# Kernel tuning notes

Hardware: AMD Instinct MI355X
Metric: run time of the kernel (lower is better)

The kernel has to match this reference:

```python
import jax, jax.numpy as jnp
import numpy as np

N_HEADS = 16
HID_DIM = 64
INPUT_DIM = 1024
B, L = 4, 1024
NEG = -10000000000.0


def setup_inputs() -> dict:
    key = jax.random.key(0)
    ks = jax.random.split(key, 10)
    d = INPUT_DIM
    h = N_HEADS * HID_DIM
    s = 1.0 / np.sqrt(d)
    return {
        "query": jax.random.normal(ks[0], (B, L, d), dtype=jnp.float32),
        "key": jax.random.normal(ks[1], (B, L, d), dtype=jnp.float32),
        "value": jax.random.normal(ks[2], (B, L, d), dtype=jnp.float32),
        "mask": jax.random.randint(ks[3], (B, 1, L, L), 0, 2, dtype=jnp.int32),
        "wq": jax.random.normal(ks[4], (d, h), dtype=jnp.float32) * s,
        "bq": jnp.zeros((h,), dtype=jnp.float32),
        "wk": jax.random.normal(ks[5], (d, h), dtype=jnp.float32) * s,
        "bk": jnp.zeros((h,), dtype=jnp.float32),
        "wv": jax.random.normal(ks[6], (d, h), dtype=jnp.float32) * s,
        "bv": jnp.zeros((h,), dtype=jnp.float32),
    }


def _split_heads(x):
    # [B, L, H*D] -> [B, H, L, D]
    b, l, _ = x.shape
    return x.reshape(b, l, N_HEADS, HID_DIM).transpose(0, 2, 1, 3)


def reference(query, key, value, mask, wq, bq, wk, bk, wv, bv):
    scale = jnp.sqrt(jnp.float32(HID_DIM))
    Q = _split_heads(query @ wq + bq)   # [B,H,L,D]
    K = _split_heads(key @ wk + bk)
    V = _split_heads(value @ wv + bv)
    energy = jnp.einsum("bhqd,bhkd->bhqk", Q, K) / scale
    energy = jnp.where(mask == 0, jnp.float32(NEG), energy)
    attention = energy  # NOTE: softmax is intentionally skipped, as in the source
    x = jnp.einsum("bhqk,bhkd->bhqd", attention, V)
    x = x.transpose(0, 2, 1, 3).reshape(query.shape[0], -1, N_HEADS * HID_DIM)
    return (attention, x)
```

## Files before the change

### kernel.cpp

```cpp
#include <hip/hip_runtime.h>
#include <stdint.h>
#include <stddef.h>


typedef __attribute__((ext_vector_type(8))) short short8;
typedef __attribute__((ext_vector_type(4))) float f32x4;
typedef __attribute__((ext_vector_type(4))) int i32x4;
typedef __attribute__((ext_vector_type(2))) unsigned int u32x2;

#define MFMA16(a, b, c) __builtin_amdgcn_mfma_f32_16x16x32_bf16(a, b, c, 0, 0, 0)

using gptr_t = const __attribute__((address_space(1))) void*;
using lptr_t = __attribute__((address_space(3))) void*;

#define NEGV -10000000000.0f
#define NEGV_BF16 0xD015u

__device__ __forceinline__ unsigned short f2bf(float f) {
  uint32_t u = __builtin_bit_cast(uint32_t, f);
  u += 0x7FFFu + ((u >> 16) & 1u);
  return (unsigned short)(u >> 16);
}

__global__ __launch_bounds__(256) void k_convert(
    const float* __restrict__ q, const float* __restrict__ k, const float* __restrict__ v,
    unsigned short* __restrict__ oq, unsigned short* __restrict__ ok,
    unsigned short* __restrict__ ov) {
  const int z = blockIdx.z;
  const float* src = z == 0 ? q : z == 1 ? k : v;
  unsigned short* dst = z == 0 ? oq : z == 1 ? ok : ov;
  const size_t idx = ((size_t)blockIdx.x * 256 + threadIdx.x) * 8;
  f32x4 a = *(const f32x4*)(src + idx);
  f32x4 b = *(const f32x4*)(src + idx + 4);
  short8 o;
  o[0] = (short)f2bf(a[0]); o[1] = (short)f2bf(a[1]);
  o[2] = (short)f2bf(a[2]); o[3] = (short)f2bf(a[3]);
  o[4] = (short)f2bf(b[0]); o[5] = (short)f2bf(b[1]);
  o[6] = (short)f2bf(b[2]); o[7] = (short)f2bf(b[3]);
  *(short8*)(dst + idx) = o;
}

__global__ __launch_bounds__(256) void k_wt(
    const float* __restrict__ wq, const float* __restrict__ wk, const float* __restrict__ wv,
    unsigned short* __restrict__ tq, unsigned short* __restrict__ tk,
    unsigned short* __restrict__ tv) {
  const int z = blockIdx.z;
  const float* src = z == 0 ? wq : z == 1 ? wk : wv;
  unsigned short* dst = z == 0 ? tq : z == 1 ? tk : tv;
  __shared__ unsigned short t[64][65];
  const int n0 = blockIdx.x * 64, k0 = blockIdx.y * 64;
#pragma unroll
  for (int i = 0; i < 16; ++i) {
    const int idx = i * 256 + threadIdx.x;
    const int r = idx >> 6, c = idx & 63;
    t[r][c] = f2bf(src[(size_t)(k0 + r) * 1024 + n0 + c]);
  }
  __syncthreads();
#pragma unroll
  for (int i = 0; i < 16; ++i) {
    const int idx = i * 256 + threadIdx.x;
    const int r = idx >> 6, c = idx & 63;
    dst[(size_t)(n0 + r) * 1024 + k0 + c] = t[c][r];
  }
}

__global__ __launch_bounds__(256) void k_gemm(
    const unsigned short* __restrict__ Xq, const unsigned short* __restrict__ Xk,
    const unsigned short* __restrict__ Xv,
    const unsigned short* __restrict__ Wq, const unsigned short* __restrict__ Wk,
    const unsigned short* __restrict__ Wv,
    const float* __restrict__ bq, const float* __restrict__ bk, const float* __restrict__ bv,
    unsigned short* __restrict__ Cq, unsigned short* __restrict__ Ck,
    unsigned short* __restrict__ Cv) {
  const int z = blockIdx.z;
  const unsigned short* X  = z == 0 ? Xq : z == 1 ? Xk : Xv;
  const unsigned short* Wt = z == 0 ? Wq : z == 1 ? Wk : Wv;
  const float* bias        = z == 0 ? bq : z == 1 ? bk : bv;
  unsigned short* C        = z == 0 ? Cq : z == 1 ? Ck : Cv;

  __shared__ unsigned short Ads[128 * 64];
  __shared__ unsigned short Bds[128 * 64];

  const int tid = threadIdx.x;
  const int w = tid >> 6, l = tid & 63;
  const int lr = l & 15, g = l >> 4;
  const int m0 = blockIdx.y * 128, n0 = blockIdx.x * 128;
  const int wm = (w >> 1) * 64, wn = (w & 1) * 64;
  const int srow = tid >> 3, sslot = tid & 7;

  f32x4 acc[4][4];
#pragma unroll
  for (int mi = 0; mi < 4; ++mi)
#pragma unroll
    for (int ni = 0; ni < 4; ++ni) acc[mi][ni] = (f32x4){0.f, 0.f, 0.f, 0.f};

  for (int kt = 0; kt < 16; ++kt) {
    const int kb = kt * 64;
#pragma unroll
    for (int i = 0; i < 4; ++i) {
      const int row = i * 32 + srow;
      const int scol = ((sslot ^ (row & 7)) << 3);
      const unsigned short* ga = X + (size_t)(m0 + row) * 1024 + kb + scol;
      const unsigned short* gb = Wt + (size_t)(n0 + row) * 1024 + kb + scol;
      __builtin_amdgcn_global_load_lds((gptr_t)ga, (lptr_t)&Ads[(i * 32 + w * 8) * 64], 16, 0, 0);
      __builtin_amdgcn_global_load_lds((gptr_t)gb, (lptr_t)&Bds[(i * 32 + w * 8) * 64], 16, 0, 0);
    }
    __syncthreads();
    short8 afr[4][2], bfr[4][2];
#pragma unroll
    for (int t = 0; t < 4; ++t)
#pragma unroll
      for (int ks = 0; ks < 2; ++ks) {
        const int ra = wm + t * 16 + lr;
        afr[t][ks] = *(const short8*)&Ads[ra * 64 + (((ks * 4 + g) ^ (ra & 7)) << 3)];
        const int rb = wn + t * 16 + lr;
        bfr[t][ks] = *(const short8*)&Bds[rb * 64 + (((ks * 4 + g) ^ (rb & 7)) << 3)];
      }
#pragma unroll
    for (int ks = 0; ks < 2; ++ks)
#pragma unroll
      for (int mi = 0; mi < 4; ++mi)
#pragma unroll
        for (int ni = 0; ni < 4; ++ni)
          acc[mi][ni] = MFMA16(afr[mi][ks], bfr[ni][ks], acc[mi][ni]);
    __syncthreads();
  }

#pragma unroll
  for (int mi = 0; mi < 4; ++mi)
#pragma unroll
    for (int ni = 0; ni < 4; ++ni) {
      const int n = n0 + wn + ni * 16 + lr;
      const float bs = bias[n];
      f32x4 a = acc[mi][ni];
#pragma unroll
      for (int r = 0; r < 4; ++r) {
        const int m = m0 + wm + mi * 16 + g * 4 + r;
        C[(size_t)m * 1024 + n] = f2bf(a[r] + bs);
      }
    }
}

__global__ __launch_bounds__(256) void k_vt(const unsigned short* __restrict__ Vb,
                                            unsigned short* __restrict__ Vt) {
  const int bh = blockIdx.y, b = bh >> 4, h = bh & 15;
  const int l0 = blockIdx.x * 64;
  __shared__ unsigned short t[64][65];
#pragma unroll
  for (int i = 0; i < 16; ++i) {
    const int idx = i * 256 + threadIdx.x;
    const int r = idx >> 6, c = idx & 63;
    t[r][c] = Vb[(size_t)(b * 1024 + l0 + r) * 1024 + h * 64 + c];
  }
  __syncthreads();
#pragma unroll
  for (int i = 0; i < 16; ++i) {
    const int idx = i * 256 + threadIdx.x;
    const int r = idx >> 6, c = idx & 63;
    Vt[(size_t)(bh * 64 + r) * 1024 + l0 + c] = t[c][r];
  }
}

__global__ __launch_bounds__(512, 4) void k_attn(
    const unsigned short* __restrict__ Qb, const unsigned short* __restrict__ Kb,
    const unsigned short* __restrict__ Vt, const int* __restrict__ mask,
    float* __restrict__ att, float* __restrict__ xout) {
  const int bh = blockIdx.y, b = bh >> 4, h = bh & 15;
  const int tid = threadIdx.x;
  const int w = tid >> 6, l = tid & 63;
  const int lr = l & 15, g = l >> 4;
  const int q0 = blockIdx.x * 128 + w * 16;

  __shared__ unsigned short Kl[128 * 64];
  __shared__ unsigned short Vl[64 * 128];
  __shared__ unsigned short Pl[8 * 16 * 128];
  unsigned short* Pw = &Pl[w * 16 * 128];

  short8 qf[2];
#pragma unroll
  for (int ks = 0; ks < 2; ++ks)
    qf[ks] = *(const short8*)&Qb[(size_t)(b * 1024 + q0 + lr) * 1024 +
                                 h * 64 + ks * 32 + g * 8];

  f32x4 xacc[4];
#pragma unroll
  for (int di = 0; di < 4; ++di) xacc[di] = (f32x4){0.f, 0.f, 0.f, 0.f};

  for (int kt = 0; kt < 8; ++kt) {
    const int kb = kt * 128;
    __syncthreads();
#pragma unroll
    for (int i = 0; i < 2; ++i) {
      const int row = i * 64 + (tid >> 3);
      const int slot = tid & 7;
      const unsigned short* src = Kb + (size_t)(b * 1024 + kb + row) * 1024 +
                                  h * 64 + ((slot ^ (row & 7)) << 3);
      __builtin_amdgcn_global_load_lds((gptr_t)src, (lptr_t)&Kl[(i * 64 + w * 8) * 64], 16, 0, 0);
    }
#pragma unroll
    for (int i = 0; i < 2; ++i) {
      const int row = i * 32 + (tid >> 4);
      const int slot = tid & 15;
      const unsigned short* src = Vt + (size_t)(bh * 64 + row) * 1024 + kb +
                                  ((slot ^ (row & 7)) << 3);
      __builtin_amdgcn_global_load_lds((gptr_t)src, (lptr_t)&Vl[(i * 32 + w * 4) * 128], 16, 0, 0);
    }
    __syncthreads();

    f32x4 s[8];
#pragma unroll
    for (int ni = 0; ni < 8; ++ni) {
      f32x4 a = (f32x4){0.f, 0.f, 0.f, 0.f};
#pragma unroll
      for (int ks = 0; ks < 2; ++ks) {
        const int row = ni * 16 + lr;
        short8 kf = *(const short8*)&Kl[row * 64 + (((ks * 4 + g) ^ (row & 7)) << 3)];
        a = MFMA16(kf, qf[ks], a);
      }
      s[ni] = a;
    }
#pragma unroll
    for (int ni = 0; ni < 8; ++ni) {
      u32x2 pk;
      pk[0] = (uint32_t)f2bf(s[ni][0] * 0.125f) | ((uint32_t)f2bf(s[ni][1] * 0.125f) << 16);
      pk[1] = (uint32_t)f2bf(s[ni][2] * 0.125f) | ((uint32_t)f2bf(s[ni][3] * 0.125f) << 16);
      const int colq = ni * 16 + g * 4;
      *(u32x2*)&Pw[lr * 128 + (colq ^ ((lr & 7) << 3))] = pk;
    }
    asm volatile("s_waitcnt lgkmcnt(0)" ::: "memory");
    __builtin_amdgcn_sched_barrier(0);
#pragma unroll
    for (int p = 0; p < 8; ++p) {
      const int flat = p * 256 + l * 4;
      const int row = flat >> 7;
      const int col = flat & 127;
      const int eb = row * 128 + (col ^ ((row & 7) << 3));
      u32x2 pr = *(const u32x2*)&Pw[eb];
      i32x4 mv = *(const i32x4*)&mask[(size_t)(b * 1024 + q0 + row) * 1024 + kb + col];
      const uint32_t u0 = pr[0], u1 = pr[1];
      f32x4 e;
      e[0] = mv[0] ? __builtin_bit_cast(float, u0 << 16) : NEGV;
      e[1] = mv[1] ? __builtin_bit_cast(float, u0 & 0xFFFF0000u) : NEGV;
      e[2] = mv[2] ? __builtin_bit_cast(float, u1 << 16) : NEGV;
      e[3] = mv[3] ? __builtin_bit_cast(float, u1 & 0xFFFF0000u) : NEGV;
      __builtin_nontemporal_store(
          e, (f32x4*)&att[(size_t)(bh * 1024 + q0 + row) * 1024 + kb + col]);
      u32x2 wb;
      wb[0] = (mv[0] ? (u0 & 0xFFFFu) : NEGV_BF16) |
              ((mv[1] ? (u0 >> 16) : NEGV_BF16) << 16);
      wb[1] = (mv[2] ? (u1 & 0xFFFFu) : NEGV_BF16) |
              ((mv[3] ? (u1 >> 16) : NEGV_BF16) << 16);
      *(u32x2*)&Pw[eb] = wb;
    }
    asm volatile("s_waitcnt lgkmcnt(0)" ::: "memory");
    __builtin_amdgcn_sched_barrier(0);
#pragma unroll
    for (int ks4 = 0; ks4 < 4; ++ks4) {
      const int colk = ks4 * 32 + g * 8;
      short8 pa = *(const short8*)&Pw[lr * 128 + (colk ^ ((lr & 7) << 3))];
#pragma unroll
      for (int di = 0; di < 4; ++di) {
        const int vr = di * 16 + lr;
        short8 vf = *(const short8*)&Vl[vr * 128 + (colk ^ ((vr & 7) << 3))];
        xacc[di] = MFMA16(pa, vf, xacc[di]);
      }
    }
    asm volatile("" ::: "memory");
  }

#pragma unroll
  for (int di = 0; di < 4; ++di) {
    f32x4 a = xacc[di];
#pragma unroll
    for (int r = 0; r < 4; ++r) {
      const int q = q0 + g * 4 + r;
      __builtin_nontemporal_store(
          a[r], &xout[(size_t)(b * 1024 + q) * 1024 + h * 64 + di * 16 + lr]);
    }
  }
}

extern "C" void kernel_launch(void* const* d_in, const int* in_sizes, int n_in,
                              void* d_out, int out_size, void* d_ws, size_t ws_size,
                              hipStream_t stream) {
  (void)in_sizes; (void)n_in; (void)out_size;
  const float* q   = (const float*)d_in[0];
  const float* k   = (const float*)d_in[1];
  const float* v   = (const float*)d_in[2];
  const int* mask  = (const int*)d_in[3];
  const float* wq  = (const float*)d_in[4];
  const float* bq  = (const float*)d_in[5];
  const float* wk  = (const float*)d_in[6];
  const float* bk  = (const float*)d_in[7];
  const float* wv  = (const float*)d_in[8];
  const float* bv  = (const float*)d_in[9];
  float* att = (float*)d_out;
  float* x   = att + (size_t)4 * 16 * 1024 * 1024;

  char* ws = (char*)d_ws;
  const size_t SZX = (size_t)4096 * 1024 * 2;
  const size_t SZW = (size_t)1024 * 1024 * 2;
  if (ws_size < 7 * SZX + 3 * SZW) return;
  unsigned short* Xq  = (unsigned short*)(ws);
  unsigned short* Xk  = (unsigned short*)(ws + SZX);
  unsigned short* Xv  = (unsigned short*)(ws + 2 * SZX);
  unsigned short* Wtq = (unsigned short*)(ws + 3 * SZX);
  unsigned short* Wtk = (unsigned short*)(ws + 3 * SZX + SZW);
  unsigned short* Wtv = (unsigned short*)(ws + 3 * SZX + 2 * SZW);
  unsigned short* Qb  = (unsigned short*)(ws + 3 * SZX + 3 * SZW);
  unsigned short* Kb  = (unsigned short*)(ws + 4 * SZX + 3 * SZW);
  unsigned short* Vb  = (unsigned short*)(ws + 5 * SZX + 3 * SZW);
  unsigned short* Vt  = (unsigned short*)(ws + 6 * SZX + 3 * SZW);

  k_convert<<<dim3(2048, 1, 3), 256, 0, stream>>>(q, k, v, Xq, Xk, Xv);
  k_wt<<<dim3(16, 16, 3), 256, 0, stream>>>(wq, wk, wv, Wtq, Wtk, Wtv);
  k_gemm<<<dim3(8, 32, 3), 256, 0, stream>>>(Xq, Xk, Xv, Wtq, Wtk, Wtv,
                                             bq, bk, bv, Qb, Kb, Vb);
  k_vt<<<dim3(16, 64), 256, 0, stream>>>(Vb, Vt);
  k_attn<<<dim3(8, 64), 512, 0, stream>>>(Qb, Kb, Vt, mask, att, x);
}
```

Baseline: 157.6 us.

## Fuse input bf16 conversion and V transpose into projection GEMM, prefetch mask

Removes the separate fp32-to-bf16 conversion kernel by loading fp32 activations directly in the GEMM and converting them while staging into LDS. The V projection epilogue now writes the transposed per-head layout directly, eliminating the k_vt transpose kernel and its intermediate buffer. In the attention kernel, mask tiles are software-prefetched into registers one key tile ahead with nontemporal loads. The cost is synchronous register-path A loads in the GEMM, which lose the async global-to-LDS path, plus extra register pressure from the mask prefetch.

```diff
diff --git a/kernel.cpp b/kernel.cpp
--- a/kernel.cpp
+++ b/kernel.cpp
@@ -20,24 +20,6 @@
   uint32_t u = __builtin_bit_cast(uint32_t, f);
   u += 0x7FFFu + ((u >> 16) & 1u);
   return (unsigned short)(u >> 16);
-}
-
-__global__ __launch_bounds__(256) void k_convert(
-    const float* __restrict__ q, const float* __restrict__ k, const float* __restrict__ v,
-    unsigned short* __restrict__ oq, unsigned short* __restrict__ ok,
-    unsigned short* __restrict__ ov) {
-  const int z = blockIdx.z;
-  const float* src = z == 0 ? q : z == 1 ? k : v;
-  unsigned short* dst = z == 0 ? oq : z == 1 ? ok : ov;
-  const size_t idx = ((size_t)blockIdx.x * 256 + threadIdx.x) * 8;
-  f32x4 a = *(const f32x4*)(src + idx);
-  f32x4 b = *(const f32x4*)(src + idx + 4);
-  short8 o;
-  o[0] = (short)f2bf(a[0]); o[1] = (short)f2bf(a[1]);
-  o[2] = (short)f2bf(a[2]); o[3] = (short)f2bf(a[3]);
-  o[4] = (short)f2bf(b[0]); o[5] = (short)f2bf(b[1]);
-  o[6] = (short)f2bf(b[2]); o[7] = (short)f2bf(b[3]);
-  *(short8*)(dst + idx) = o;
 }
 
 __global__ __launch_bounds__(256) void k_wt(
@@ -65,18 +47,17 @@
 }
 
 __global__ __launch_bounds__(256) void k_gemm(
-    const unsigned short* __restrict__ Xq, const unsigned short* __restrict__ Xk,
-    const unsigned short* __restrict__ Xv,
+    const float* __restrict__ Xq, const float* __restrict__ Xk,
+    const float* __restrict__ Xv,
     const unsigned short* __restrict__ Wq, const unsigned short* __restrict__ Wk,
     const unsigned short* __restrict__ Wv,
     const float* __restrict__ bq, const float* __restrict__ bk, const float* __restrict__ bv,
     unsigned short* __restrict__ Cq, unsigned short* __restrict__ Ck,
-    unsigned short* __restrict__ Cv) {
+    unsigned short* __restrict__ Vt) {
   const int z = blockIdx.z;
-  const unsigned short* X  = z == 0 ? Xq : z == 1 ? Xk : Xv;
+  const float* X           = z == 0 ? Xq : z == 1 ? Xk : Xv;
   const unsigned short* Wt = z == 0 ? Wq : z == 1 ? Wk : Wv;
   const float* bias        = z == 0 ? bq : z == 1 ? bk : bv;
-  unsigned short* C        = z == 0 ? Cq : z == 1 ? Ck : Cv;
 
   __shared__ unsigned short Ads[128 * 64];
   __shared__ unsigned short Bds[128 * 64];
@@ -98,11 +79,23 @@
     const int kb = kt * 64;
 #pragma unroll
     for (int i = 0; i < 4; ++i) {
+      const int idx = i * 256 + tid;
+      const int row = idx >> 3, c8 = idx & 7;
+      const float* ga = X + (size_t)(m0 + row) * 1024 + kb + c8 * 8;
+      f32x4 a0 = *(const f32x4*)ga;
+      f32x4 a1 = *(const f32x4*)(ga + 4);
+      short8 pk;
+      pk[0] = (short)f2bf(a0[0]); pk[1] = (short)f2bf(a0[1]);
+      pk[2] = (short)f2bf(a0[2]); pk[3] = (short)f2bf(a0[3]);
+      pk[4] = (short)f2bf(a1[0]); pk[5] = (short)f2bf(a1[1]);
+      pk[6] = (short)f2bf(a1[2]); pk[7] = (short)f2bf(a1[3]);
+      *(short8*)&Ads[row * 64 + ((c8 ^ (row & 7)) << 3)] = pk;
+    }
+#pragma unroll
+    for (int i = 0; i < 4; ++i) {
       const int row = i * 32 + srow;
       const int scol = ((sslot ^ (row & 7)) << 3);
-      const unsigned short* ga = X + (size_t)(m0 + row) * 1024 + kb + scol;
       const unsigned short* gb = Wt + (size_t)(n0 + row) * 1024 + kb + scol;
-      __builtin_amdgcn_global_load_lds((gptr_t)ga, (lptr_t)&Ads[(i * 32 + w * 8) * 64], 16, 0, 0);
       __builtin_amdgcn_global_load_lds((gptr_t)gb, (lptr_t)&Bds[(i * 32 + w * 8) * 64], 16, 0, 0);
     }
     __syncthreads();
@@ -126,38 +119,38 @@
     __syncthreads();
   }
 
-#pragma unroll
-  for (int mi = 0; mi < 4; ++mi)
-#pragma unroll
-    for (int ni = 0; ni < 4; ++ni) {
-      const int n = n0 + wn + ni * 16 + lr;
-      const float bs = bias[n];
-      f32x4 a = acc[mi][ni];
-#pragma unroll
-      for (int r = 0; r < 4; ++r) {
-        const int m = m0 + wm + mi * 16 + g * 4 + r;
-        C[(size_t)m * 1024 + n] = f2bf(a[r] + bs);
-      }
-    }
-}
-
-__global__ __launch_bounds__(256) void k_vt(const unsigned short* __restrict__ Vb,
-                                            unsigned short* __restrict__ Vt) {
-  const int bh = blockIdx.y, b = bh >> 4, h = bh & 15;
-  const int l0 = blockIdx.x * 64;
-  __shared__ unsigned short t[64][65];
-#pragma unroll
-  for (int i = 0; i < 16; ++i) {
-    const int idx = i * 256 + threadIdx.x;
-    const int r = idx >> 6, c = idx & 63;
-    t[r][c] = Vb[(size_t)(b * 1024 + l0 + r) * 1024 + h * 64 + c];
-  }
-  __syncthreads();
-#pragma unroll
-  for (int i = 0; i < 16; ++i) {
-    const int idx = i * 256 + threadIdx.x;
-    const int r = idx >> 6, c = idx & 63;
-    Vt[(size_t)(bh * 64 + r) * 1024 + l0 + c] = t[c][r];
+  if (z != 2) {
+    unsigned short* C = z == 0 ? Cq : Ck;
+#pragma unroll
+    for (int mi = 0; mi < 4; ++mi)
+#pragma unroll
+      for (int ni = 0; ni < 4; ++ni) {
+        const int n = n0 + wn + ni * 16 + lr;
+        const float bs = bias[n];
+        f32x4 a = acc[mi][ni];
+#pragma unroll
+        for (int r = 0; r < 4; ++r) {
+          const int m = m0 + wm + mi * 16 + g * 4 + r;
+          C[(size_t)m * 1024 + n] = f2bf(a[r] + bs);
+        }
+      }
+  } else {
+#pragma unroll
+    for (int mi = 0; mi < 4; ++mi)
+#pragma unroll
+      for (int ni = 0; ni < 4; ++ni) {
+        const int ng = n0 + wn + ni * 16 + lr;
+        const int hh = ng >> 6, dd = ng & 63;
+        const float bs = bias[ng];
+        f32x4 a = acc[mi][ni];
+        const int mg = m0 + wm + mi * 16 + g * 4;
+        const int bb = mg >> 10;
+        const int ll = mg & 1023;
+        u32x2 pk;
+        pk[0] = (uint32_t)f2bf(a[0] + bs) | ((uint32_t)f2bf(a[1] + bs) << 16);
+        pk[1] = (uint32_t)f2bf(a[2] + bs) | ((uint32_t)f2bf(a[3] + bs) << 16);
+        *(u32x2*)&Vt[(size_t)((bb * 16 + hh) * 64 + dd) * 1024 + ll] = pk;
+      }
   }
 }
 
@@ -186,6 +179,15 @@
 #pragma unroll
   for (int di = 0; di < 4; ++di) xacc[di] = (f32x4){0.f, 0.f, 0.f, 0.f};
 
+  i32x4 mnext[8];
+#pragma unroll
+  for (int p = 0; p < 8; ++p) {
+    const int flat = p * 256 + l * 4;
+    const int row = flat >> 7, col = flat & 127;
+    mnext[p] = __builtin_nontemporal_load(
+        (const i32x4*)&mask[(size_t)(b * 1024 + q0 + row) * 1024 + col]);
+  }
+
   for (int kt = 0; kt < 8; ++kt) {
     const int kb = kt * 128;
     __syncthreads();
@@ -236,7 +238,7 @@
       const int col = flat & 127;
       const int eb = row * 128 + (col ^ ((row & 7) << 3));
       u32x2 pr = *(const u32x2*)&Pw[eb];
-      i32x4 mv = *(const i32x4*)&mask[(size_t)(b * 1024 + q0 + row) * 1024 + kb + col];
+      const i32x4 mv = mnext[p];
       const uint32_t u0 = pr[0], u1 = pr[1];
       f32x4 e;
       e[0] = mv[0] ? __builtin_bit_cast(float, u0 << 16) : NEGV;
@@ -251,6 +253,14 @@
       wb[1] = (mv[2] ? (u1 & 0xFFFFu) : NEGV_BF16) |
               ((mv[3] ? (u1 >> 16) : NEGV_BF16) << 16);
       *(u32x2*)&Pw[eb] = wb;
+    }
+    const int kbn = (kt == 7) ? kb : kb + 128;
+#pragma unroll
+    for (int p = 0; p < 8; ++p) {
+      const int flat = p * 256 + l * 4;
+      const int row = flat >> 7, col = flat & 127;
+      mnext[p] = __builtin_nontemporal_load(
+          (const i32x4*)&mask[(size_t)(b * 1024 + q0 + row) * 1024 + kbn + col]);
     }
     asm volatile("s_waitcnt lgkmcnt(0)" ::: "memory");
     __builtin_amdgcn_sched_barrier(0);
@@ -300,22 +310,16 @@
   char* ws = (char*)d_ws;
   const size_t SZX = (size_t)4096 * 1024 * 2;
   const size_t SZW = (size_t)1024 * 1024 * 2;
-  if (ws_size < 7 * SZX + 3 * SZW) return;
-  unsigned short* Xq  = (unsigned short*)(ws);
-  unsigned short* Xk  = (unsigned short*)(ws + SZX);
-  unsigned short* Xv  = (unsigned short*)(ws + 2 * SZX);
-  unsigned short* Wtq = (unsigned short*)(ws + 3 * SZX);
-  unsigned short* Wtk = (unsigned short*)(ws + 3 * SZX + SZW);
-  unsigned short* Wtv = (unsigned short*)(ws + 3 * SZX + 2 * SZW);
-  unsigned short* Qb  = (unsigned short*)(ws + 3 * SZX + 3 * SZW);
-  unsigned short* Kb  = (unsigned short*)(ws + 4 * SZX + 3 * SZW);
-  unsigned short* Vb  = (unsigned short*)(ws + 5 * SZX + 3 * SZW);
-  unsigned short* Vt  = (unsigned short*)(ws + 6 * SZX + 3 * SZW);
-
-  k_convert<<<dim3(2048, 1, 3), 256, 0, stream>>>(q, k, v, Xq, Xk, Xv);
+  if (ws_size < 3 * SZX + 3 * SZW) return;
+  unsigned short* Wtq = (unsigned short*)(ws);
+  unsigned short* Wtk = (unsigned short*)(ws + SZW);
+  unsigned short* Wtv = (unsigned short*)(ws + 2 * SZW);
+  unsigned short* Qb  = (unsigned short*)(ws + 3 * SZW);
+  unsigned short* Kb  = (unsigned short*)(ws + 3 * SZW + SZX);
+  unsigned short* Vt  = (unsigned short*)(ws + 3 * SZW + 2 * SZX);
+
   k_wt<<<dim3(16, 16, 3), 256, 0, stream>>>(wq, wk, wv, Wtq, Wtk, Wtv);
-  k_gemm<<<dim3(8, 32, 3), 256, 0, stream>>>(Xq, Xk, Xv, Wtq, Wtk, Wtv,
-                                             bq, bk, bv, Qb, Kb, Vb);
-  k_vt<<<dim3(16, 64), 256, 0, stream>>>(Vb, Vt);
+  k_gemm<<<dim3(8, 32, 3), 256, 0, stream>>>(q, k, v, Wtq, Wtk, Wtv,
+                                             bq, bk, bv, Qb, Kb, Vt);
   k_attn<<<dim3(8, 64), 512, 0, stream>>>(Qb, Kb, Vt, mask, att, x);
 }
```

Result: slower. 268.9 us (+70.6%).

## Fuse V transpose into GEMM epilogue and restructure attention tiling

Applied to the files above, without the earlier changes.

The GEMM epilogue for the V projection now writes V directly in transposed per-head layout, which removes the separate k_vt kernel and its workspace buffer. Both GEMM and attention use a 1D grid with a remapped block index that spreads work round-robin across the eight XCDs for better L2 locality. Attention blocks shrink from 512 to 256 threads (64 queries per block, occupancy hint raised to 5) and process each 128-key tile in two halves. V fragments are read straight from global memory instead of being staged in LDS, and mask loads are issued before the QK MFMAs to hide their latency. The trade-off is more uncoalesced global reads of V and scattered 8-byte stores in the GEMM epilogue.

```diff
diff --git a/kernel.cpp b/kernel.cpp
--- a/kernel.cpp
+++ b/kernel.cpp
@@ -71,12 +71,13 @@
     const unsigned short* __restrict__ Wv,
     const float* __restrict__ bq, const float* __restrict__ bk, const float* __restrict__ bv,
     unsigned short* __restrict__ Cq, unsigned short* __restrict__ Ck,
-    unsigned short* __restrict__ Cv) {
-  const int z = blockIdx.z;
+    unsigned short* __restrict__ Vt) {
+  const int bid = blockIdx.x;
+  const int wg = (bid & 7) * 96 + (bid >> 3);
+  const int z = wg >> 8, rem = wg & 255;
   const unsigned short* X  = z == 0 ? Xq : z == 1 ? Xk : Xv;
   const unsigned short* Wt = z == 0 ? Wq : z == 1 ? Wk : Wv;
   const float* bias        = z == 0 ? bq : z == 1 ? bk : bv;
-  unsigned short* C        = z == 0 ? Cq : z == 1 ? Ck : Cv;
 
   __shared__ unsigned short Ads[128 * 64];
   __shared__ unsigned short Bds[128 * 64];
@@ -84,7 +85,7 @@
   const int tid = threadIdx.x;
   const int w = tid >> 6, l = tid & 63;
   const int lr = l & 15, g = l >> 4;
-  const int m0 = blockIdx.y * 128, n0 = blockIdx.x * 128;
+  const int m0 = (rem >> 3) * 128, n0 = (rem & 7) * 128;
   const int wm = (w >> 1) * 64, wn = (w & 1) * 64;
   const int srow = tid >> 3, sslot = tid & 7;
 
@@ -126,55 +127,56 @@
     __syncthreads();
   }
 
-#pragma unroll
-  for (int mi = 0; mi < 4; ++mi)
-#pragma unroll
-    for (int ni = 0; ni < 4; ++ni) {
-      const int n = n0 + wn + ni * 16 + lr;
-      const float bs = bias[n];
-      f32x4 a = acc[mi][ni];
-#pragma unroll
-      for (int r = 0; r < 4; ++r) {
-        const int m = m0 + wm + mi * 16 + g * 4 + r;
-        C[(size_t)m * 1024 + n] = f2bf(a[r] + bs);
-      }
-    }
-}
-
-__global__ __launch_bounds__(256) void k_vt(const unsigned short* __restrict__ Vb,
-                                            unsigned short* __restrict__ Vt) {
-  const int bh = blockIdx.y, b = bh >> 4, h = bh & 15;
-  const int l0 = blockIdx.x * 64;
-  __shared__ unsigned short t[64][65];
-#pragma unroll
-  for (int i = 0; i < 16; ++i) {
-    const int idx = i * 256 + threadIdx.x;
-    const int r = idx >> 6, c = idx & 63;
-    t[r][c] = Vb[(size_t)(b * 1024 + l0 + r) * 1024 + h * 64 + c];
-  }
-  __syncthreads();
-#pragma unroll
-  for (int i = 0; i < 16; ++i) {
-    const int idx = i * 256 + threadIdx.x;
-    const int r = idx >> 6, c = idx & 63;
-    Vt[(size_t)(bh * 64 + r) * 1024 + l0 + c] = t[c][r];
-  }
-}
-
-__global__ __launch_bounds__(512, 4) void k_attn(
+  if (z != 2) {
+    unsigned short* C = z == 0 ? Cq : Ck;
+#pragma unroll
+    for (int mi = 0; mi < 4; ++mi)
+#pragma unroll
+      for (int ni = 0; ni < 4; ++ni) {
+        const int n = n0 + wn + ni * 16 + lr;
+        const float bs = bias[n];
+        f32x4 a = acc[mi][ni];
+#pragma unroll
+        for (int r = 0; r < 4; ++r) {
+          const int m = m0 + wm + mi * 16 + g * 4 + r;
+          C[(size_t)m * 1024 + n] = f2bf(a[r] + bs);
+        }
+      }
+  } else {
+#pragma unroll
+    for (int mi = 0; mi < 4; ++mi)
+#pragma unroll
+      for (int ni = 0; ni < 4; ++ni) {
+        const int ng = n0 + wn + ni * 16 + lr;
+        const int hh = ng >> 6, dd = ng & 63;
+        const float bs = bias[ng];
+        f32x4 a = acc[mi][ni];
+        const int mg = m0 + wm + mi * 16 + g * 4;
+        const int bb = mg >> 10, ll = mg & 1023;
+        u32x2 pk;
+        pk[0] = (uint32_t)f2bf(a[0] + bs) | ((uint32_t)f2bf(a[1] + bs) << 16);
+        pk[1] = (uint32_t)f2bf(a[2] + bs) | ((uint32_t)f2bf(a[3] + bs) << 16);
+        *(u32x2*)&Vt[(size_t)((bb * 16 + hh) * 64 + dd) * 1024 + ll] = pk;
+      }
+  }
+}
+
+__global__ __launch_bounds__(256, 5) void k_attn(
     const unsigned short* __restrict__ Qb, const unsigned short* __restrict__ Kb,
     const unsigned short* __restrict__ Vt, const int* __restrict__ mask,
     float* __restrict__ att, float* __restrict__ xout) {
-  const int bh = blockIdx.y, b = bh >> 4, h = bh & 15;
+  const int bid = blockIdx.x;
+  const int wg = (bid & 7) * 128 + (bid >> 3);
+  const int bh = wg >> 4, qt = wg & 15;
+  const int b = bh >> 4, h = bh & 15;
   const int tid = threadIdx.x;
   const int w = tid >> 6, l = tid & 63;
   const int lr = l & 15, g = l >> 4;
-  const int q0 = blockIdx.x * 128 + w * 16;
+  const int q0 = qt * 64 + w * 16;
 
   __shared__ unsigned short Kl[128 * 64];
-  __shared__ unsigned short Vl[64 * 128];
-  __shared__ unsigned short Pl[8 * 16 * 128];
-  unsigned short* Pw = &Pl[w * 16 * 128];
+  __shared__ unsigned short Pl[4][16 * 128];
+  unsigned short* Pw = Pl[w];
 
   short8 qf[2];
 #pragma unroll
@@ -190,79 +192,77 @@
     const int kb = kt * 128;
     __syncthreads();
 #pragma unroll
-    for (int i = 0; i < 2; ++i) {
-      const int row = i * 64 + (tid >> 3);
+    for (int i = 0; i < 4; ++i) {
+      const int row = i * 32 + (tid >> 3);
       const int slot = tid & 7;
       const unsigned short* src = Kb + (size_t)(b * 1024 + kb + row) * 1024 +
                                   h * 64 + ((slot ^ (row & 7)) << 3);
-      __builtin_amdgcn_global_load_lds((gptr_t)src, (lptr_t)&Kl[(i * 64 + w * 8) * 64], 16, 0, 0);
-    }
-#pragma unroll
-    for (int i = 0; i < 2; ++i) {
-      const int row = i * 32 + (tid >> 4);
-      const int slot = tid & 15;
-      const unsigned short* src = Vt + (size_t)(bh * 64 + row) * 1024 + kb +
-                                  ((slot ^ (row & 7)) << 3);
-      __builtin_amdgcn_global_load_lds((gptr_t)src, (lptr_t)&Vl[(i * 32 + w * 4) * 128], 16, 0, 0);
+      __builtin_amdgcn_global_load_lds((gptr_t)src, (lptr_t)&Kl[(i * 32 + w * 8) * 64], 16, 0, 0);
     }
     __syncthreads();
 
-    f32x4 s[8];
-#pragma unroll
-    for (int ni = 0; ni < 8; ++ni) {
-      f32x4 a = (f32x4){0.f, 0.f, 0.f, 0.f};
-#pragma unroll
-      for (int ks = 0; ks < 2; ++ks) {
-        const int row = ni * 16 + lr;
-        short8 kf = *(const short8*)&Kl[row * 64 + (((ks * 4 + g) ^ (row & 7)) << 3)];
-        a = MFMA16(kf, qf[ks], a);
-      }
-      s[ni] = a;
-    }
-#pragma unroll
-    for (int ni = 0; ni < 8; ++ni) {
-      u32x2 pk;
-      pk[0] = (uint32_t)f2bf(s[ni][0] * 0.125f) | ((uint32_t)f2bf(s[ni][1] * 0.125f) << 16);
-      pk[1] = (uint32_t)f2bf(s[ni][2] * 0.125f) | ((uint32_t)f2bf(s[ni][3] * 0.125f) << 16);
-      const int colq = ni * 16 + g * 4;
-      *(u32x2*)&Pw[lr * 128 + (colq ^ ((lr & 7) << 3))] = pk;
-    }
-    asm volatile("s_waitcnt lgkmcnt(0)" ::: "memory");
-    __builtin_amdgcn_sched_barrier(0);
-#pragma unroll
-    for (int p = 0; p < 8; ++p) {
-      const int flat = p * 256 + l * 4;
-      const int row = flat >> 7;
-      const int col = flat & 127;
-      const int eb = row * 128 + (col ^ ((row & 7) << 3));
-      u32x2 pr = *(const u32x2*)&Pw[eb];
-      i32x4 mv = *(const i32x4*)&mask[(size_t)(b * 1024 + q0 + row) * 1024 + kb + col];
-      const uint32_t u0 = pr[0], u1 = pr[1];
-      f32x4 e;
-      e[0] = mv[0] ? __builtin_bit_cast(float, u0 << 16) : NEGV;
-      e[1] = mv[1] ? __builtin_bit_cast(float, u0 & 0xFFFF0000u) : NEGV;
-      e[2] = mv[2] ? __builtin_bit_cast(float, u1 << 16) : NEGV;
-      e[3] = mv[3] ? __builtin_bit_cast(float, u1 & 0xFFFF0000u) : NEGV;
-      __builtin_nontemporal_store(
-          e, (f32x4*)&att[(size_t)(bh * 1024 + q0 + row) * 1024 + kb + col]);
-      u32x2 wb;
-      wb[0] = (mv[0] ? (u0 & 0xFFFFu) : NEGV_BF16) |
-              ((mv[1] ? (u0 >> 16) : NEGV_BF16) << 16);
-      wb[1] = (mv[2] ? (u1 & 0xFFFFu) : NEGV_BF16) |
-              ((mv[3] ? (u1 >> 16) : NEGV_BF16) << 16);
-      *(u32x2*)&Pw[eb] = wb;
-    }
-    asm volatile("s_waitcnt lgkmcnt(0)" ::: "memory");
-    __builtin_amdgcn_sched_barrier(0);
-#pragma unroll
-    for (int ks4 = 0; ks4 < 4; ++ks4) {
-      const int colk = ks4 * 32 + g * 8;
-      short8 pa = *(const short8*)&Pw[lr * 128 + (colk ^ ((lr & 7) << 3))];
-#pragma unroll
-      for (int di = 0; di < 4; ++di) {
-        const int vr = di * 16 + lr;
-        short8 vf = *(const short8*)&Vl[vr * 128 + (colk ^ ((vr & 7) << 3))];
-        xacc[di] = MFMA16(pa, vf, xacc[di]);
+#pragma unroll
+    for (int hh = 0; hh < 2; ++hh) {
+      i32x4 mv[4];
+#pragma unroll
+      for (int p = 0; p < 4; ++p)
+        mv[p] = *(const i32x4*)&mask[(size_t)(b * 1024 + q0 + p * 4 + g) * 1024 +
+                                     kb + hh * 64 + lr * 4];
+      f32x4 s[4];
+#pragma unroll
+      for (int n2 = 0; n2 < 4; ++n2) {
+        const int row = (hh * 4 + n2) * 16 + lr;
+        f32x4 a = (f32x4){0.f, 0.f, 0.f, 0.f};
+#pragma unroll
+        for (int ks = 0; ks < 2; ++ks) {
+          short8 kf = *(const short8*)&Kl[row * 64 + (((ks * 4 + g) ^ (row & 7)) << 3)];
+          a = MFMA16(kf, qf[ks], a);
+        }
+        s[n2] = a;
+      }
+#pragma unroll
+      for (int n2 = 0; n2 < 4; ++n2) {
+        u32x2 pk;
+        pk[0] = (uint32_t)f2bf(s[n2][0] * 0.125f) | ((uint32_t)f2bf(s[n2][1] * 0.125f) << 16);
+        pk[1] = (uint32_t)f2bf(s[n2][2] * 0.125f) | ((uint32_t)f2bf(s[n2][3] * 0.125f) << 16);
+        const int colq = (hh * 4 + n2) * 16 + g * 4;
+        *(u32x2*)&Pw[lr * 128 + (colq ^ ((lr & 7) << 3))] = pk;
+      }
+      asm volatile("s_waitcnt lgkmcnt(0)" ::: "memory");
+      __builtin_amdgcn_sched_barrier(0);
+#pragma unroll
+      for (int p = 0; p < 4; ++p) {
+        const int row = p * 4 + g;
+        const int col = hh * 64 + lr * 4;
+        const int eb = row * 128 + (col ^ ((row & 7) << 3));
+        u32x2 pr = *(const u32x2*)&Pw[eb];
+        const uint32_t u0 = pr[0], u1 = pr[1];
+        f32x4 e;
+        e[0] = mv[p][0] ? __builtin_bit_cast(float, u0 << 16) : NEGV;
+        e[1] = mv[p][1] ? __builtin_bit_cast(float, u0 & 0xFFFF0000u) : NEGV;
+        e[2] = mv[p][2] ? __builtin_bit_cast(float, u1 << 16) : NEGV;
+        e[3] = mv[p][3] ? __builtin_bit_cast(float, u1 & 0xFFFF0000u) : NEGV;
+        __builtin_nontemporal_store(
+            e, (f32x4*)&att[(size_t)(bh * 1024 + q0 + row) * 1024 + kb + col]);
+        u32x2 wb;
+        wb[0] = (mv[p][0] ? (u0 & 0xFFFFu) : NEGV_BF16) |
+                ((mv[p][1] ? (u0 >> 16) : NEGV_BF16) << 16);
+        wb[1] = (mv[p][2] ? (u1 & 0xFFFFu) : NEGV_BF16) |
+                ((mv[p][3] ? (u1 >> 16) : NEGV_BF16) << 16);
+        *(u32x2*)&Pw[eb] = wb;
+      }
+      asm volatile("s_waitcnt lgkmcnt(0)" ::: "memory");
+      __builtin_amdgcn_sched_barrier(0);
+#pragma unroll
+      for (int k2 = 0; k2 < 2; ++k2) {
+        const int colk = (hh * 2 + k2) * 32 + g * 8;
+        short8 pa = *(const short8*)&Pw[lr * 128 + (colk ^ ((lr & 7) << 3))];
+#pragma unroll
+        for (int di = 0; di < 4; ++di) {
+          short8 vf = *(const short8*)&Vt[(size_t)(bh * 64 + di * 16 + lr) * 1024 +
+                                          kb + colk];
+          xacc[di] = MFMA16(pa, vf, xacc[di]);
+        }
       }
     }
     asm volatile("" ::: "memory");
@@ -300,7 +300,7 @@
   char* ws = (char*)d_ws;
   const size_t SZX = (size_t)4096 * 1024 * 2;
   const size_t SZW = (size_t)1024 * 1024 * 2;
-  if (ws_size < 7 * SZX + 3 * SZW) return;
+  if (ws_size < 6 * SZX + 3 * SZW) return;
   unsigned short* Xq  = (unsigned short*)(ws);
   unsigned short* Xk  = (unsigned short*)(ws + SZX);
   unsigned short* Xv  = (unsigned short*)(ws + 2 * SZX);
@@ -309,13 +309,11 @@
   unsigned short* Wtv = (unsigned short*)(ws + 3 * SZX + 2 * SZW);
   unsigned short* Qb  = (unsigned short*)(ws + 3 * SZX + 3 * SZW);
   unsigned short* Kb  = (unsigned short*)(ws + 4 * SZX + 3 * SZW);
-  unsigned short* Vb  = (unsigned short*)(ws + 5 * SZX + 3 * SZW);
-  unsigned short* Vt  = (unsigned short*)(ws + 6 * SZX + 3 * SZW);
+  unsigned short* Vt  = (unsigned short*)(ws + 5 * SZX + 3 * SZW);
 
   k_convert<<<dim3(2048, 1, 3), 256, 0, stream>>>(q, k, v, Xq, Xk, Xv);
   k_wt<<<dim3(16, 16, 3), 256, 0, stream>>>(wq, wk, wv, Wtq, Wtk, Wtv);
-  k_gemm<<<dim3(8, 32, 3), 256, 0, stream>>>(Xq, Xk, Xv, Wtq, Wtk, Wtv,
-                                             bq, bk, bv, Qb, Kb, Vb);
-  k_vt<<<dim3(16, 64), 256, 0, stream>>>(Vb, Vt);
-  k_attn<<<dim3(8, 64), 512, 0, stream>>>(Qb, Kb, Vt, mask, att, x);
-}
+  k_gemm<<<dim3(768), 256, 0, stream>>>(Xq, Xk, Xv, Wtq, Wtk, Wtv,
+                                        bq, bk, bv, Qb, Kb, Vt);
+  k_attn<<<dim3(1024), 256, 0, stream>>>(Qb, Kb, Vt, mask, att, x);
+}
```

Result: slower. 207.4 us (+31.6%).

## Fuse V transpose into GEMM epilogue and remap blocks across XCDs

Applied to the files above, without the earlier changes.

Removes the separate k_vt transpose kernel by having the V-projection GEMM write its bf16 output directly in transposed [B,H,D,L] layout with packed 4-element stores. Both the GEMM and attention kernels switch to a 1D grid whose block index is permuted so neighbouring tiles land on the same XCD, aiming for better L2 locality. This saves one launch and a full round trip of the V buffer. The transposed stores from the GEMM are strided across rows and may coalesce poorly.

```diff
diff --git a/kernel.cpp b/kernel.cpp
--- a/kernel.cpp
+++ b/kernel.cpp
@@ -71,12 +71,13 @@
     const unsigned short* __restrict__ Wv,
     const float* __restrict__ bq, const float* __restrict__ bk, const float* __restrict__ bv,
     unsigned short* __restrict__ Cq, unsigned short* __restrict__ Ck,
-    unsigned short* __restrict__ Cv) {
-  const int z = blockIdx.z;
+    unsigned short* __restrict__ Vt) {
+  const int bid = blockIdx.x;
+  const int wg = (bid & 7) * 96 + (bid >> 3);
+  const int z = wg >> 8, rem = wg & 255;
   const unsigned short* X  = z == 0 ? Xq : z == 1 ? Xk : Xv;
   const unsigned short* Wt = z == 0 ? Wq : z == 1 ? Wk : Wv;
   const float* bias        = z == 0 ? bq : z == 1 ? bk : bv;
-  unsigned short* C        = z == 0 ? Cq : z == 1 ? Ck : Cv;
 
   __shared__ unsigned short Ads[128 * 64];
   __shared__ unsigned short Bds[128 * 64];
@@ -84,7 +85,7 @@
   const int tid = threadIdx.x;
   const int w = tid >> 6, l = tid & 63;
   const int lr = l & 15, g = l >> 4;
-  const int m0 = blockIdx.y * 128, n0 = blockIdx.x * 128;
+  const int m0 = (rem >> 3) * 128, n0 = (rem & 7) * 128;
   const int wm = (w >> 1) * 64, wn = (w & 1) * 64;
   const int srow = tid >> 3, sslot = tid & 7;
 
@@ -126,38 +127,37 @@
     __syncthreads();
   }
 
-#pragma unroll
-  for (int mi = 0; mi < 4; ++mi)
-#pragma unroll
-    for (int ni = 0; ni < 4; ++ni) {
-      const int n = n0 + wn + ni * 16 + lr;
-      const float bs = bias[n];
-      f32x4 a = acc[mi][ni];
-#pragma unroll
-      for (int r = 0; r < 4; ++r) {
-        const int m = m0 + wm + mi * 16 + g * 4 + r;
-        C[(size_t)m * 1024 + n] = f2bf(a[r] + bs);
-      }
-    }
-}
-
-__global__ __launch_bounds__(256) void k_vt(const unsigned short* __restrict__ Vb,
-                                            unsigned short* __restrict__ Vt) {
-  const int bh = blockIdx.y, b = bh >> 4, h = bh & 15;
-  const int l0 = blockIdx.x * 64;
-  __shared__ unsigned short t[64][65];
-#pragma unroll
-  for (int i = 0; i < 16; ++i) {
-    const int idx = i * 256 + threadIdx.x;
-    const int r = idx >> 6, c = idx & 63;
-    t[r][c] = Vb[(size_t)(b * 1024 + l0 + r) * 1024 + h * 64 + c];
-  }
-  __syncthreads();
-#pragma unroll
-  for (int i = 0; i < 16; ++i) {
-    const int idx = i * 256 + threadIdx.x;
-    const int r = idx >> 6, c = idx & 63;
-    Vt[(size_t)(bh * 64 + r) * 1024 + l0 + c] = t[c][r];
+  if (z != 2) {
+    unsigned short* C = z == 0 ? Cq : Ck;
+#pragma unroll
+    for (int mi = 0; mi < 4; ++mi)
+#pragma unroll
+      for (int ni = 0; ni < 4; ++ni) {
+        const int n = n0 + wn + ni * 16 + lr;
+        const float bs = bias[n];
+        f32x4 a = acc[mi][ni];
+#pragma unroll
+        for (int r = 0; r < 4; ++r) {
+          const int m = m0 + wm + mi * 16 + g * 4 + r;
+          C[(size_t)m * 1024 + n] = f2bf(a[r] + bs);
+        }
+      }
+  } else {
+#pragma unroll
+    for (int mi = 0; mi < 4; ++mi)
+#pragma unroll
+      for (int ni = 0; ni < 4; ++ni) {
+        const int ng = n0 + wn + ni * 16 + lr;
+        const int hh = ng >> 6, dd = ng & 63;
+        const float bs = bias[ng];
+        f32x4 a = acc[mi][ni];
+        const int mg = m0 + wm + mi * 16 + g * 4;
+        const int bb = mg >> 10, ll = mg & 1023;
+        u32x2 pk;
+        pk[0] = (uint32_t)f2bf(a[0] + bs) | ((uint32_t)f2bf(a[1] + bs) << 16);
+        pk[1] = (uint32_t)f2bf(a[2] + bs) | ((uint32_t)f2bf(a[3] + bs) << 16);
+        *(u32x2*)&Vt[(size_t)((bb * 16 + hh) * 64 + dd) * 1024 + ll] = pk;
+      }
   }
 }
 
@@ -165,11 +165,14 @@
     const unsigned short* __restrict__ Qb, const unsigned short* __restrict__ Kb,
     const unsigned short* __restrict__ Vt, const int* __restrict__ mask,
     float* __restrict__ att, float* __restrict__ xout) {
-  const int bh = blockIdx.y, b = bh >> 4, h = bh & 15;
+  const int bid = blockIdx.x;
+  const int wg = (bid & 7) * 64 + (bid >> 3);
+  const int bh = wg >> 3, qt = wg & 7;
+  const int b = bh >> 4, h = bh & 15;
   const int tid = threadIdx.x;
   const int w = tid >> 6, l = tid & 63;
   const int lr = l & 15, g = l >> 4;
-  const int q0 = blockIdx.x * 128 + w * 16;
+  const int q0 = qt * 128 + w * 16;
 
   __shared__ unsigned short Kl[128 * 64];
   __shared__ unsigned short Vl[64 * 128];
@@ -300,7 +303,7 @@
   char* ws = (char*)d_ws;
   const size_t SZX = (size_t)4096 * 1024 * 2;
   const size_t SZW = (size_t)1024 * 1024 * 2;
-  if (ws_size < 7 * SZX + 3 * SZW) return;
+  if (ws_size < 6 * SZX + 3 * SZW) return;
   unsigned short* Xq  = (unsigned short*)(ws);
   unsigned short* Xk  = (unsigned short*)(ws + SZX);
   unsigned short* Xv  = (unsigned short*)(ws + 2 * SZX);
@@ -309,13 +312,11 @@
   unsigned short* Wtv = (unsigned short*)(ws + 3 * SZX + 2 * SZW);
   unsigned short* Qb  = (unsigned short*)(ws + 3 * SZX + 3 * SZW);
   unsigned short* Kb  = (unsigned short*)(ws + 4 * SZX + 3 * SZW);
-  unsigned short* Vb  = (unsigned short*)(ws + 5 * SZX + 3 * SZW);
-  unsigned short* Vt  = (unsigned short*)(ws + 6 * SZX + 3 * SZW);
+  unsigned short* Vt  = (unsigned short*)(ws + 5 * SZX + 3 * SZW);
 
   k_convert<<<dim3(2048, 1, 3), 256, 0, stream>>>(q, k, v, Xq, Xk, Xv);
   k_wt<<<dim3(16, 16, 3), 256, 0, stream>>>(wq, wk, wv, Wtq, Wtk, Wtv);
-  k_gemm<<<dim3(8, 32, 3), 256, 0, stream>>>(Xq, Xk, Xv, Wtq, Wtk, Wtv,
-                                             bq, bk, bv, Qb, Kb, Vb);
-  k_vt<<<dim3(16, 64), 256, 0, stream>>>(Vb, Vt);
-  k_attn<<<dim3(8, 64), 512, 0, stream>>>(Qb, Kb, Vt, mask, att, x);
-}
+  k_gemm<<<dim3(768), 256, 0, stream>>>(Xq, Xk, Xv, Wtq, Wtk, Wtv,
+                                        bq, bk, bv, Qb, Kb, Vt);
+  k_attn<<<dim3(512), 512, 0, stream>>>(Qb, Kb, Vt, mask, att, x);
+}
```

Result: faster. 147.7 us (median of 3 runs) (-6.3%).
